# Optimization experiments

Hardware: AMD Instinct MI355X
Metric: run time of the kernel (lower is better)

## Reference

```python
import jax, jax.numpy as jnp
import numpy as np

P = 2        # patch_size
HEADS = 1


def _conv(x, w, b, groups=1):
    # NCHW conv, kernel 3x3, SAME padding (stride 1)
    y = jax.lax.conv_general_dilated(
        x, w, window_strides=(1, 1), padding='SAME',
        dimension_numbers=('NCHW', 'OIHW', 'NCHW'),
        feature_group_count=groups)
    return y + b[None, :, None, None]


def _unfold(x, p):
    # torch.nn.Unfold(kernel=p, stride=p): [B,C,h,w] -> [B, C*p*p, n]
    B, C, h, w = x.shape
    x = x.reshape(B, C, h // p, p, w // p, p)
    x = x.transpose(0, 1, 3, 5, 2, 4)  # (B, C, ph, pw, h/p, w/p)
    return x.reshape(B, C * p * p, (h // p) * (w // p))


def _fold(x, p, h, w):
    # inverse of _unfold (non-overlapping patches)
    B = x.shape[0]
    C = x.shape[1] // (p * p)
    x = x.reshape(B, C, p, p, h // p, w // p)
    x = x.transpose(0, 1, 4, 2, 5, 3)  # (B, C, h/p, ph, w/p, pw)
    return x.reshape(B, C, h, w)


def setup_inputs() -> dict:
    key = jax.random.key(0)
    ks = jax.random.split(key, 9)
    c = 64
    x = jax.random.normal(ks[0], (2, 5, c, 64, 64), jnp.float32)
    wq = jax.random.normal(ks[1], (c, 1, 3, 3), jnp.float32) * 0.1
    bq = jax.random.normal(ks[2], (c,), jnp.float32) * 0.1
    wk = jax.random.normal(ks[3], (c, 1, 3, 3), jnp.float32) * 0.1
    bk = jax.random.normal(ks[4], (c,), jnp.float32) * 0.1
    wv = jax.random.normal(ks[5], (c, c, 3, 3), jnp.float32) * 0.05
    bv = jax.random.normal(ks[6], (c,), jnp.float32) * 0.1
    wc = jax.random.normal(ks[7], (c, c, 3, 3), jnp.float32) * 0.05
    bc = jax.random.normal(ks[8], (c,), jnp.float32) * 0.1
    return {"x": x, "wq": wq, "bq": bq, "wk": wk, "bk": bk,
            "wv": wv, "bv": bv, "wc": wc, "bc": bc}


def reference(x, wq, bq, wk, bk, wv, bv, wc, bc):
    b, t, c, h, w = x.shape
    p, H = P, HEADS
    D = p * p * c           # 256
    d = D // H              # per-head dim
    n = (h // p) * (w // p)  # tokens per frame

    xf = x.reshape(b * t, c, h, w)
    q = _conv(xf, wq, bq, groups=c)   # depthwise
    k = _conv(xf, wk, bk, groups=c)   # depthwise
    v = _conv(xf, wv, bv)             # dense conv

    def to_tokens(y):
        # [bt, D, n] -> [b, H, d, t*n]
        u = _unfold(y, p).reshape(b, t, H, d, n)
        return u.transpose(0, 2, 3, 1, 4).reshape(b, H, d, t * n)

    uq, uk, uv = to_tokens(q), to_tokens(k), to_tokens(v)

    attn = jnp.einsum('bhdi,bhdj->bhij', uq, uk) * (d ** -0.5)
    attn = jax.nn.softmax(attn, axis=-1)           # [b,H,tn,tn]
    ax = jnp.einsum('bhij,bhdj->bhid', attn, uv)   # [b,H,tn,d]

    ax = ax.reshape(b, H, t, n, d).transpose(0, 2, 1, 4, 3).reshape(b * t, D, n)
    feat = _fold(ax, p, h, w)                      # [bt, c, h, w]
    out = _conv(feat, wc, bc).reshape(x.shape) + x
    return out
```

## Files before the change

kernel.cpp:

```cpp
#include <hip/hip_runtime.h>
#include <hip/hip_bf16.h>

typedef __attribute__((ext_vector_type(8))) short short8;
typedef __attribute__((ext_vector_type(8))) unsigned short ushort8;
typedef __attribute__((ext_vector_type(4))) unsigned short ushort4v;
typedef __attribute__((ext_vector_type(4))) float f32x4;

#define NTOK 5120
#define DDIM 256
#define NJC 8

__device__ __forceinline__ unsigned short f2bf(float f) {
  union { float f; unsigned int u; } x; x.f = f;
  unsigned int r = x.u + 0x7FFFu + ((x.u >> 16) & 1u);
  return (unsigned short)(r >> 16);
}
__device__ __forceinline__ float bf2f(unsigned short u) {
  union { unsigned int i; float f; } x; x.i = ((unsigned int)u) << 16; return x.f;
}

__global__ __launch_bounds__(256) void qk_gen(
    const float* __restrict__ xin, const float* __restrict__ wq,
    const float* __restrict__ bq, const float* __restrict__ wk,
    const float* __restrict__ bk, unsigned short* __restrict__ qt,
    unsigned short* __restrict__ kt)
{
  const int ch = blockIdx.x;
  const int bt = blockIdx.y;
  const int b = bt / 5, tf = bt % 5;
  const int tid = threadIdx.x;
  const float* xp = xin + ((size_t)bt * 64 + ch) * 4096;
  float wqv[9], wkv[9];
  #pragma unroll
  for (int i = 0; i < 9; i++) { wqv[i] = wq[ch * 9 + i]; wkv[i] = wk[ch * 9 + i]; }
  const float bqv = bq[ch], bkv = bk[ch];

  #pragma unroll
  for (int p = 0; p < 4; p++) {
    int pid = tid + p * 256;
    int gy = pid >> 5, gx = pid & 31;
    float v[4][4];
    #pragma unroll
    for (int r = 0; r < 4; r++) {
      int yy = 2 * gy - 1 + r;
      #pragma unroll
      for (int cc = 0; cc < 4; cc++) {
        int xx = 2 * gx - 1 + cc;
        bool ok = (yy >= 0) && (yy < 64) && (xx >= 0) && (xx < 64);
        v[r][cc] = ok ? xp[yy * 64 + xx] : 0.f;
      }
    }
    unsigned short qo[4], ko[4];
    #pragma unroll
    for (int py = 0; py < 2; py++)
      #pragma unroll
      for (int px = 0; px < 2; px++) {
        float aq = bqv, ak = bkv;
        #pragma unroll
        for (int dy = 0; dy < 3; dy++)
          #pragma unroll
          for (int dx = 0; dx < 3; dx++) {
            float xv = v[py + dy][px + dx];
            aq += wqv[dy * 3 + dx] * xv;
            ak += wkv[dy * 3 + dx] * xv;
          }
        qo[py * 2 + px] = f2bf(aq);
        ko[py * 2 + px] = f2bf(ak);
      }
    size_t base = ((size_t)(b * NTOK + tf * 1024 + pid)) * DDIM + ch * 4;
    ushort4v qv = { qo[0], qo[1], qo[2], qo[3] };
    ushort4v kv = { ko[0], ko[1], ko[2], ko[3] };
    *(ushort4v*)(qt + base) = qv;
    *(ushort4v*)(kt + base) = kv;
  }
}

__global__ __launch_bounds__(256) void wt_gen(
    const float* __restrict__ w0, const float* __restrict__ w1,
    unsigned short* __restrict__ o0, unsigned short* __restrict__ o1)
{
  const int tap = blockIdx.x;
  const float* src = blockIdx.y ? w1 : w0;
  unsigned short* dst = blockIdx.y ? o1 : o0;
  const int t = threadIdx.x;
  #pragma unroll
  for (int i = 0; i < 16; i++) {
    int oi = t + i * 256;
    dst[tap * 4096 + oi] = f2bf(src[(size_t)oi * 9 + tap]);
  }
}

template<int MODE>
__global__ __launch_bounds__(256) void conv_mfma(
    const float* __restrict__ src, const unsigned short* __restrict__ wt,
    const float* __restrict__ bias, const float* __restrict__ resid,
    float* __restrict__ dstf, unsigned short* __restrict__ vt)
{
  const int strip = blockIdx.x;
  const int bt = blockIdx.y;
  const int y0 = strip * 2;
  const int tid = threadIdx.x;
  const int sw = tid >> 6, lane = tid & 63;
  const int ry = sw >> 1, ch = sw & 1;
  const int g = lane >> 4, c = lane & 15;

  __shared__ __align__(16) unsigned short lds_in[4 * 66 * 64];
  __shared__ __align__(16) unsigned short lds_w[64 * 64];

  {
    const int rr = lane >> 4;
    const int cb = lane & 15;
    const int row = y0 - 1 + rr;
    const bool rok = (row >= 0) && (row < 64);
    #pragma unroll
    for (int pp = 0; pp < 8; ++pp) {
      const int ci0 = sw * 16 + pp * 2;
      f32x4 va = { 0.f, 0.f, 0.f, 0.f }, vb = { 0.f, 0.f, 0.f, 0.f };
      if (rok) {
        va = *(const f32x4*)(src + ((size_t)(bt * 64 + ci0)) * 4096 + row * 64 + cb * 4);
        vb = *(const f32x4*)(src + ((size_t)(bt * 64 + ci0 + 1)) * 4096 + row * 64 + cb * 4);
      }
      char* rbase = (char*)lds_in + (rr * 66) * 128 + (ci0 & 7) * 2;
      const int sl = ci0 >> 3;
      #pragma unroll
      for (int q = 0; q < 4; ++q) {
        int lcol = cb * 4 + q + 1;
        unsigned int pk = (unsigned int)f2bf(va[q]) | ((unsigned int)f2bf(vb[q]) << 16);
        *(unsigned int*)(rbase + lcol * 128 + ((sl ^ (lcol & 7)) * 16)) = pk;
      }
      if (cb == 0)  *(unsigned int*)(rbase + ((sl ^ 0) * 16)) = 0u;
      if (cb == 15) *(unsigned int*)(rbase + 65 * 128 + ((sl ^ 1) * 16)) = 0u;
    }
  }

  f32x4 acc[2][4];
  #pragma unroll
  for (int ct = 0; ct < 2; ct++)
    #pragma unroll
    for (int xt = 0; xt < 4; xt++) acc[ct][xt] = (f32x4){ 0.f, 0.f, 0.f, 0.f };

  #pragma unroll 1
  for (int tap = 0; tap < 9; ++tap) {
    __syncthreads();
    {
      const unsigned short* wp = wt + tap * 4096;
      #pragma unroll
      for (int h = 0; h < 2; ++h) {
        int el = h * 2048 + tid * 8;
        int co = el >> 6, sl = (el & 63) >> 3;
        short8 wv8 = *(const short8*)(wp + el);
        *(short8*)((char*)lds_w + co * 128 + ((sl ^ (co & 7)) * 16)) = wv8;
      }
    }
    __syncthreads();
    const int dy = tap / 3 - 1, dx = tap % 3 - 1;
    const int rowp = ry + 1 + dy;
    #pragma unroll
    for (int kblk = 0; kblk < 2; ++kblk) {
      short8 af[2], bf[4];
      #pragma unroll
      for (int ct = 0; ct < 2; ++ct) {
        int co = ch * 32 + ct * 16 + c;
        af[ct] = *(const short8*)((char*)lds_w + co * 128 + (((kblk * 4 + g) ^ (co & 7)) * 16));
      }
      #pragma unroll
      for (int xt = 0; xt < 4; ++xt) {
        int lcol = xt * 16 + c + dx + 1;
        bf[xt] = *(const short8*)((char*)lds_in + (rowp * 66 + lcol) * 128 + (((kblk * 4 + g) ^ (lcol & 7)) * 16));
      }
      #pragma unroll
      for (int ct = 0; ct < 2; ++ct)
        #pragma unroll
        for (int xt = 0; xt < 4; ++xt)
          acc[ct][xt] = __builtin_amdgcn_mfma_f32_16x16x32_bf16(af[ct], bf[xt], acc[ct][xt], 0, 0, 0);
    }
  }

  const int y = y0 + ry;
  if (MODE == 0) {
    const int b = bt / 5, tf = bt % 5;
    const int py = y & 1, gy = y >> 1;
    #pragma unroll
    for (int ct = 0; ct < 2; ++ct)
      #pragma unroll
      for (int r = 0; r < 4; ++r) {
        const int co = ch * 32 + ct * 16 + g * 4 + r;
        const float bv = bias[co];
        #pragma unroll
        for (int xt = 0; xt < 4; ++xt) {
          int x = xt * 16 + c;
          int d = co * 4 + py * 2 + (x & 1);
          int tok = tf * 1024 + gy * 32 + (x >> 1);
          vt[((size_t)(b * DDIM + d)) * NTOK + tok] = f2bf(acc[ct][xt][r] + bv);
        }
      }
  } else {
    #pragma unroll
    for (int ct = 0; ct < 2; ++ct)
      #pragma unroll
      for (int r = 0; r < 4; ++r) {
        const int co = ch * 32 + ct * 16 + g * 4 + r;
        const float bv = bias[co];
        const size_t rowb = ((size_t)(bt * 64 + co)) * 4096 + (size_t)y * 64;
        #pragma unroll
        for (int xt = 0; xt < 4; ++xt) {
          int x = xt * 16 + c;
          dstf[rowb + x] = acc[ct][xt][r] + bv + resid[rowb + x];
        }
      }
  }
}

__global__ __launch_bounds__(256) void attn_kernel(
    const unsigned short* __restrict__ qt, const unsigned short* __restrict__ kt,
    const unsigned short* __restrict__ vt, float* __restrict__ po,
    float* __restrict__ pm, float* __restrict__ pl)
{
  const int wgid = blockIdx.x;
  const int chunk = wgid / 320;
  const int within = wgid % 320;
  const int slice = chunk * 8 + (within & 7);
  const int b = slice >> 3;
  const int jc = slice & 7;
  const int i0 = (within >> 3) * 128;
  const int jchunk = NTOK / NJC;
  const int tid = threadIdx.x;
  const int w = tid >> 6, lane = tid & 63;
  const int g = lane >> 4, c = lane & 15;

  __shared__ __align__(16) unsigned short lds_k[64 * 256];
  __shared__ __align__(16) unsigned short lds_v[256 * 64];

  short8 qf[2][8];
  #pragma unroll
  for (int st = 0; st < 2; st++) {
    const unsigned short* qr = qt + ((size_t)(b * NTOK + i0 + w * 32 + st * 16 + c)) * DDIM + g * 8;
    #pragma unroll
    for (int kb = 0; kb < 8; kb++) qf[st][kb] = *(const short8*)(qr + kb * 32);
  }
  f32x4 o[32];
  #pragma unroll
  for (int i = 0; i < 32; i++) o[i] = (f32x4){ 0.f, 0.f, 0.f, 0.f };
  float m[2][4], l[2][4];
  #pragma unroll
  for (int st = 0; st < 2; st++)
    #pragma unroll
    for (int r = 0; r < 4; r++) { m[st][r] = -1e30f; l[st][r] = 0.f; }

  const int sr = tid >> 5, sc = tid & 31;
  const int vdr = tid >> 3, vcc = tid & 7;
  char* pb = (char*)lds_k + w * 4096;

  const int jbeg = jc * jchunk;
  for (int j0 = jbeg; j0 < jbeg + jchunk; j0 += 64) {
    #pragma unroll
    for (int p = 0; p < 8; p++) {
      int row = sr + p * 8;
      short8 kv = *(const short8*)(kt + ((size_t)(b * NTOK + j0 + row)) * DDIM + sc * 8);
      *(short8*)((char*)lds_k + row * 512 + ((sc ^ (row & 7)) * 16)) = kv;
    }
    #pragma unroll
    for (int p = 0; p < 8; p++) {
      int dd = vdr + p * 32;
      short8 vv = *(const short8*)(vt + ((size_t)(b * DDIM + dd)) * NTOK + j0 + vcc * 8);
      *(short8*)((char*)lds_v + dd * 128 + ((vcc ^ (dd & 7)) * 16)) = vv;
    }
    __syncthreads();

    f32x4 s0[4], s1[4];
    #pragma unroll
    for (int js = 0; js < 4; js++) {
      s0[js] = (f32x4){ 0.f, 0.f, 0.f, 0.f };
      s1[js] = (f32x4){ 0.f, 0.f, 0.f, 0.f };
      int row = js * 16 + c;
      int sw2 = row & 7;
      #pragma unroll
      for (int kb = 0; kb < 8; kb++) {
        short8 kf = *(const short8*)((char*)lds_k + row * 512 + (((kb * 4 + g) ^ sw2) * 16));
        s0[js] = __builtin_amdgcn_mfma_f32_16x16x32_bf16(qf[0][kb], kf, s0[js], 0, 0, 0);
        s1[js] = __builtin_amdgcn_mfma_f32_16x16x32_bf16(qf[1][kb], kf, s1[js], 0, 0, 0);
      }
    }
    float pvv[4][4], alpha[4];
    #pragma unroll
    for (int r = 0; r < 4; r++) {
      float mx = fmaxf(fmaxf(s0[0][r], s0[1][r]), fmaxf(s0[2][r], s0[3][r])) * 0.0625f;
      #pragma unroll
      for (int off = 1; off < 16; off <<= 1) mx = fmaxf(mx, __shfl_xor(mx, off));
      float mn = fmaxf(m[0][r], mx);
      alpha[r] = __expf(m[0][r] - mn);
      float p0 = __expf(s0[0][r] * 0.0625f - mn);
      float p1 = __expf(s0[1][r] * 0.0625f - mn);
      float p2 = __expf(s0[2][r] * 0.0625f - mn);
      float p3 = __expf(s0[3][r] * 0.0625f - mn);
      pvv[0][r] = p0; pvv[1][r] = p1; pvv[2][r] = p2; pvv[3][r] = p3;
      float sum = p0 + p1 + p2 + p3;
      #pragma unroll
      for (int off = 1; off < 16; off <<= 1) sum += __shfl_xor(sum, off);
      l[0][r] = l[0][r] * alpha[r] + sum;
      m[0][r] = mn;
    }
    {
      f32x4 av = { alpha[0], alpha[1], alpha[2], alpha[3] };
      #pragma unroll
      for (int ds = 0; ds < 16; ds++) o[ds] *= av;
    }
    __syncthreads();
    #pragma unroll
    for (int js = 0; js < 4; js++)
      #pragma unroll
      for (int r = 0; r < 4; r++) {
        int row = 4 * g + r;
        int slot = (js * 2 + (c >> 3)) ^ (row & 7);
        *(unsigned short*)(pb + row * 128 + slot * 16 + (c & 7) * 2) = f2bf(pvv[js][r]);
      }
    #pragma unroll
    for (int r = 0; r < 4; r++) {
      float mx = fmaxf(fmaxf(s1[0][r], s1[1][r]), fmaxf(s1[2][r], s1[3][r])) * 0.0625f;
      #pragma unroll
      for (int off = 1; off < 16; off <<= 1) mx = fmaxf(mx, __shfl_xor(mx, off));
      float mn = fmaxf(m[1][r], mx);
      alpha[r] = __expf(m[1][r] - mn);
      float p0 = __expf(s1[0][r] * 0.0625f - mn);
      float p1 = __expf(s1[1][r] * 0.0625f - mn);
      float p2 = __expf(s1[2][r] * 0.0625f - mn);
      float p3 = __expf(s1[3][r] * 0.0625f - mn);
      pvv[0][r] = p0; pvv[1][r] = p1; pvv[2][r] = p2; pvv[3][r] = p3;
      float sum = p0 + p1 + p2 + p3;
      #pragma unroll
      for (int off = 1; off < 16; off <<= 1) sum += __shfl_xor(sum, off);
      l[1][r] = l[1][r] * alpha[r] + sum;
      m[1][r] = mn;
    }
    {
      f32x4 av = { alpha[0], alpha[1], alpha[2], alpha[3] };
      #pragma unroll
      for (int ds = 0; ds < 16; ds++) o[16 + ds] *= av;
    }
    #pragma unroll
    for (int js = 0; js < 4; js++)
      #pragma unroll
      for (int r = 0; r < 4; r++) {
        int row = 16 + 4 * g + r;
        int slot = (js * 2 + (c >> 3)) ^ (row & 7);
        *(unsigned short*)(pb + row * 128 + slot * 16 + (c & 7) * 2) = f2bf(pvv[js][r]);
      }
    short8 pf[2][2];
    #pragma unroll
    for (int st = 0; st < 2; st++)
      #pragma unroll
      for (int k2 = 0; k2 < 2; k2++)
        pf[st][k2] = *(short8*)(pb + (st * 16 + c) * 128 + (((k2 * 4 + g) ^ (c & 7)) * 16));
    #pragma unroll
    for (int ds = 0; ds < 16; ds++) {
      int vrow = ds * 16 + c;
      int sw2 = c & 7;
      #pragma unroll
      for (int k2 = 0; k2 < 2; k2++) {
        short8 vf = *(const short8*)((char*)lds_v + vrow * 128 + (((k2 * 4 + g) ^ sw2) * 16));
        o[ds]      = __builtin_amdgcn_mfma_f32_16x16x32_bf16(pf[0][k2], vf, o[ds], 0, 0, 0);
        o[16 + ds] = __builtin_amdgcn_mfma_f32_16x16x32_bf16(pf[1][k2], vf, o[16 + ds], 0, 0, 0);
      }
    }
    __syncthreads();
  }
  #pragma unroll
  for (int st = 0; st < 2; st++) {
    const size_t rbase = ((size_t)(b * NJC + jc)) * NTOK + i0 + w * 32 + st * 16;
    #pragma unroll
    for (int ds = 0; ds < 16; ds++)
      #pragma unroll
      for (int r = 0; r < 4; r++)
        po[(rbase + 4 * g + r) * DDIM + ds * 16 + c] = o[st * 16 + ds][r];
    if (c == 0) {
      #pragma unroll
      for (int r = 0; r < 4; r++) {
        pm[rbase + 4 * g + r] = m[st][r];
        pl[rbase + 4 * g + r] = l[st][r];
      }
    }
  }
}

__global__ __launch_bounds__(256) void attn_combine(
    const float* __restrict__ po, const float* __restrict__ pm,
    const float* __restrict__ pl, float* __restrict__ feat, int njc)
{
  const int b = blockIdx.y;
  const int i0 = blockIdx.x * 64;
  const int t = threadIdx.x;
  const int row = t >> 2, dq = (t & 3) * 64;
  const int i = i0 + row;

  float M = -1e30f, L = 0.f;
  f32x4 acc[16];
  #pragma unroll
  for (int q = 0; q < 16; q++) acc[q] = (f32x4){ 0.f, 0.f, 0.f, 0.f };

  #pragma unroll 1
  for (int jc = 0; jc < njc; jc++) {
    const size_t rb = ((size_t)(b * njc + jc)) * NTOK + i;
    float mj = pm[rb], lj = pl[rb];
    float mn = fmaxf(M, mj);
    float so = __expf(M - mn), sn = __expf(mj - mn);
    const float* pp = po + rb * DDIM + dq;
    #pragma unroll
    for (int q = 0; q < 16; q++) {
      f32x4 v = *(const f32x4*)(pp + q * 4);
      acc[q] = acc[q] * so + v * sn;
    }
    L = L * so + lj * sn;
    M = mn;
  }
  const float inv = 1.f / L;
  const int tf = i >> 10, jn = i & 1023;
  const int gy = jn >> 5, gx = jn & 31;
  const size_t fb = ((size_t)((b * 5 + tf) * 64)) * 4096 + (2 * gy) * 64 + 2 * gx;
  #pragma unroll
  for (int q = 0; q < 16; q++) {
    f32x4 a = acc[q] * inv;
    int ch = (dq + q * 4) >> 2;
    size_t base = fb + (size_t)ch * 4096;
    feat[base] = a[0]; feat[base + 1] = a[1];
    feat[base + 64] = a[2]; feat[base + 65] = a[3];
  }
}

extern "C" void kernel_launch(void* const* d_in, const int* in_sizes, int n_in,
                              void* d_out, int out_size, void* d_ws, size_t ws_size,
                              hipStream_t stream) {
  const float* x  = (const float*)d_in[0];
  const float* wq = (const float*)d_in[1];
  const float* bq = (const float*)d_in[2];
  const float* wk = (const float*)d_in[3];
  const float* bk = (const float*)d_in[4];
  const float* wv = (const float*)d_in[5];
  const float* bv = (const float*)d_in[6];
  const float* wc = (const float*)d_in[7];
  const float* bc = (const float*)d_in[8];
  float* out = (float*)d_out;

  char* ws = (char*)d_ws;
  unsigned short* qt = (unsigned short*)(ws);
  unsigned short* kt = (unsigned short*)(ws + 5242880);
  unsigned short* vt = (unsigned short*)(ws + 10485760);
  float*          ft = (float*)(ws + 15728640);
  unsigned short* wtv = (unsigned short*)(ws + 26214400);
  unsigned short* wtc = (unsigned short*)(ws + 26288128);
  const size_t big_off = 26361856;
  float* po = (float*)(ws + big_off);

  size_t po_bytes = (size_t)2 * NJC * NTOK * DDIM * 4;
  float* pm = (float*)(ws + big_off + po_bytes);
  float* pl = pm + (size_t)2 * NJC * NTOK;

  wt_gen        <<<dim3(9, 2), 256, 0, stream>>>(wv, wc, wtv, wtc);
  qk_gen        <<<dim3(64, 10), 256, 0, stream>>>(x, wq, bq, wk, bk, qt, kt);
  conv_mfma<0>  <<<dim3(32, 10), 256, 0, stream>>>(x, wtv, bv, nullptr, nullptr, vt);
  attn_kernel   <<<dim3(640), 256, 0, stream>>>(qt, kt, vt, po, pm, pl);
  attn_combine  <<<dim3(80, 2), 256, 0, stream>>>(po, pm, pl, ft, NJC);
  conv_mfma<1>  <<<dim3(32, 10), 256, 0, stream>>>(ft, wtc, bc, x, out, nullptr);
}
```

Measured before the change: 251.0 us.

## Use 512-thread attention blocks sharing K/V tiles, skip unneeded rescales

Each attention workgroup now has 8 waves covering 256 query rows instead of 4 waves covering 128, so every K/V tile staged in LDS serves twice as many queries and global K/V traffic per query is halved. The output rescale by alpha is skipped when no row max changed in the wave, which saves vector multiplies on most iterations. The P-tile writes for both sub-tiles are merged after a single barrier. In exchange the grid shrinks to 320 blocks, which may balance poorly across CUs, and a 512-thread block may hurt occupancy given the large accumulator register footprint.

```diff
diff --git a/kernel.cpp b/kernel.cpp
--- a/kernel.cpp
+++ b/kernel.cpp
@@ -211,18 +211,18 @@
   }
 }
 
-__global__ __launch_bounds__(256) void attn_kernel(
+__global__ __launch_bounds__(512) void attn_kernel(
     const unsigned short* __restrict__ qt, const unsigned short* __restrict__ kt,
     const unsigned short* __restrict__ vt, float* __restrict__ po,
     float* __restrict__ pm, float* __restrict__ pl)
 {
   const int wgid = blockIdx.x;
-  const int chunk = wgid / 320;
-  const int within = wgid % 320;
+  const int chunk = wgid / 160;
+  const int within = wgid % 160;
   const int slice = chunk * 8 + (within & 7);
   const int b = slice >> 3;
   const int jc = slice & 7;
-  const int i0 = (within >> 3) * 128;
+  const int i0 = (within >> 3) * 256;
   const int jchunk = NTOK / NJC;
   const int tid = threadIdx.x;
   const int w = tid >> 6, lane = tid & 63;
@@ -254,14 +254,14 @@
   const int jbeg = jc * jchunk;
   for (int j0 = jbeg; j0 < jbeg + jchunk; j0 += 64) {
     #pragma unroll
-    for (int p = 0; p < 8; p++) {
-      int row = sr + p * 8;
+    for (int p = 0; p < 4; p++) {
+      int row = sr + p * 16;
       short8 kv = *(const short8*)(kt + ((size_t)(b * NTOK + j0 + row)) * DDIM + sc * 8);
       *(short8*)((char*)lds_k + row * 512 + ((sc ^ (row & 7)) * 16)) = kv;
     }
     #pragma unroll
-    for (int p = 0; p < 8; p++) {
-      int dd = vdr + p * 32;
+    for (int p = 0; p < 4; p++) {
+      int dd = vdr + p * 64;
       short8 vv = *(const short8*)(vt + ((size_t)(b * DDIM + dd)) * NTOK + j0 + vcc * 8);
       *(short8*)((char*)lds_v + dd * 128 + ((vcc ^ (dd & 7)) * 16)) = vv;
     }
@@ -281,69 +281,69 @@
         s1[js] = __builtin_amdgcn_mfma_f32_16x16x32_bf16(qf[1][kb], kf, s1[js], 0, 0, 0);
       }
     }
-    float pvv[4][4], alpha[4];
+    float pvv0[4][4], pvv1[4][4], alpha[4];
+    int need;
+    need = 0;
     #pragma unroll
     for (int r = 0; r < 4; r++) {
       float mx = fmaxf(fmaxf(s0[0][r], s0[1][r]), fmaxf(s0[2][r], s0[3][r])) * 0.0625f;
       #pragma unroll
       for (int off = 1; off < 16; off <<= 1) mx = fmaxf(mx, __shfl_xor(mx, off));
-      float mn = fmaxf(m[0][r], mx);
-      alpha[r] = __expf(m[0][r] - mn);
+      float mold = m[0][r];
+      float mn = fmaxf(mold, mx);
+      alpha[r] = __expf(mold - mn);
+      if (mn > mold) need = 1;
       float p0 = __expf(s0[0][r] * 0.0625f - mn);
       float p1 = __expf(s0[1][r] * 0.0625f - mn);
       float p2 = __expf(s0[2][r] * 0.0625f - mn);
       float p3 = __expf(s0[3][r] * 0.0625f - mn);
-      pvv[0][r] = p0; pvv[1][r] = p1; pvv[2][r] = p2; pvv[3][r] = p3;
+      pvv0[0][r] = p0; pvv0[1][r] = p1; pvv0[2][r] = p2; pvv0[3][r] = p3;
       float sum = p0 + p1 + p2 + p3;
       #pragma unroll
       for (int off = 1; off < 16; off <<= 1) sum += __shfl_xor(sum, off);
       l[0][r] = l[0][r] * alpha[r] + sum;
       m[0][r] = mn;
     }
-    {
+    if (__any(need)) {
       f32x4 av = { alpha[0], alpha[1], alpha[2], alpha[3] };
       #pragma unroll
       for (int ds = 0; ds < 16; ds++) o[ds] *= av;
     }
-    __syncthreads();
-    #pragma unroll
-    for (int js = 0; js < 4; js++)
-      #pragma unroll
-      for (int r = 0; r < 4; r++) {
-        int row = 4 * g + r;
-        int slot = (js * 2 + (c >> 3)) ^ (row & 7);
-        *(unsigned short*)(pb + row * 128 + slot * 16 + (c & 7) * 2) = f2bf(pvv[js][r]);
-      }
+    need = 0;
     #pragma unroll
     for (int r = 0; r < 4; r++) {
       float mx = fmaxf(fmaxf(s1[0][r], s1[1][r]), fmaxf(s1[2][r], s1[3][r])) * 0.0625f;
       #pragma unroll
       for (int off = 1; off < 16; off <<= 1) mx = fmaxf(mx, __shfl_xor(mx, off));
-      float mn = fmaxf(m[1][r], mx);
-      alpha[r] = __expf(m[1][r] - mn);
+      float mold = m[1][r];
+      float mn = fmaxf(mold, mx);
+      alpha[r] = __expf(mold - mn);
+      if (mn > mold) need = 1;
       float p0 = __expf(s1[0][r] * 0.0625f - mn);
       float p1 = __expf(s1[1][r] * 0.0625f - mn);
       float p2 = __expf(s1[2][r] * 0.0625f - mn);
       float p3 = __expf(s1[3][r] * 0.0625f - mn);
-      pvv[0][r] = p0; pvv[1][r] = p1; pvv[2][r] = p2; pvv[3][r] = p3;
+      pvv1[0][r] = p0; pvv1[1][r] = p1; pvv1[2][r] = p2; pvv1[3][r] = p3;
       float sum = p0 + p1 + p2 + p3;
       #pragma unroll
       for (int off = 1; off < 16; off <<= 1) sum += __shfl_xor(sum, off);
       l[1][r] = l[1][r] * alpha[r] + sum;
       m[1][r] = mn;
     }
-    {
+    if (__any(need)) {
       f32x4 av = { alpha[0], alpha[1], alpha[2], alpha[3] };
       #pragma unroll
       for (int ds = 0; ds < 16; ds++) o[16 + ds] *= av;
     }
+    __syncthreads();
     #pragma unroll
     for (int js = 0; js < 4; js++)
       #pragma unroll
       for (int r = 0; r < 4; r++) {
-        int row = 16 + 4 * g + r;
+        int row = 4 * g + r;
         int slot = (js * 2 + (c >> 3)) ^ (row & 7);
-        *(unsigned short*)(pb + row * 128 + slot * 16 + (c & 7) * 2) = f2bf(pvv[js][r]);
+        *(unsigned short*)(pb + row * 128 + slot * 16 + (c & 7) * 2) = f2bf(pvv0[js][r]);
+        *(unsigned short*)(pb + (16 + row) * 128 + slot * 16 + (c & 7) * 2) = f2bf(pvv1[js][r]);
       }
     short8 pf[2][2];
     #pragma unroll
@@ -457,7 +457,7 @@
   wt_gen        <<<dim3(9, 2), 256, 0, stream>>>(wv, wc, wtv, wtc);
   qk_gen        <<<dim3(64, 10), 256, 0, stream>>>(x, wq, bq, wk, bk, qt, kt);
   conv_mfma<0>  <<<dim3(32, 10), 256, 0, stream>>>(x, wtv, bv, nullptr, nullptr, vt);
-  attn_kernel   <<<dim3(640), 256, 0, stream>>>(qt, kt, vt, po, pm, pl);
+  attn_kernel   <<<dim3(320), 512, 0, stream>>>(qt, kt, vt, po, pm, pl);
   attn_combine  <<<dim3(80, 2), 256, 0, stream>>>(po, pm, pl, ft, NJC);
   conv_mfma<1>  <<<dim3(32, 10), 256, 0, stream>>>(ft, wtc, bc, x, out, nullptr);
 }
```

After: 374.9 us. 1.49x slower.
